# Performance work log

Hardware: AMD Instinct MI355X
Metric: run time of the kernel (lower is better)

The kernel has to match this reference:

```python
import jax, jax.numpy as jnp
import numpy as np

LATENT = 3
HIDDEN = 16
INP = LATENT + 1  # prev_z cat action
B = 1048576


def setup_inputs() -> dict:
    key = jax.random.key(0)
    ks = jax.random.split(key, 11)
    s_ih = 1.0 / np.sqrt(HIDDEN)
    return {
        "prev_z": jax.random.normal(ks[0], (B, LATENT), jnp.float32),
        "action": jax.random.normal(ks[1], (B, 1), jnp.float32),
        "prev_h": jax.random.normal(ks[2], (B, HIDDEN), jnp.float32),
        # GRUCell params (torch layout: [3*H, in] and [3*H, H], gate order r,z,n)
        "W_ih": jax.random.uniform(ks[3], (3 * HIDDEN, INP), jnp.float32, -s_ih, s_ih),
        "W_hh": jax.random.uniform(ks[4], (3 * HIDDEN, HIDDEN), jnp.float32, -s_ih, s_ih),
        "b_ih": jax.random.uniform(ks[5], (3 * HIDDEN,), jnp.float32, -s_ih, s_ih),
        "b_hh": jax.random.uniform(ks[6], (3 * HIDDEN,), jnp.float32, -s_ih, s_ih),
        # prior heads
        "W_mu": jax.random.uniform(ks[7], (LATENT, HIDDEN), jnp.float32, -s_ih, s_ih),
        "b_mu": jax.random.uniform(ks[8], (LATENT,), jnp.float32, -s_ih, s_ih),
        "W_lv": jax.random.uniform(ks[9], (LATENT, HIDDEN), jnp.float32, -s_ih, s_ih),
        "b_lv": jax.random.uniform(ks[10], (LATENT,), jnp.float32, -s_ih, s_ih),
    }


def reference(prev_z, action, prev_h, W_ih, W_hh, b_ih, b_hh, W_mu, b_mu, W_lv, b_lv):
    x = jnp.concatenate([prev_z, action], axis=-1)              # [B, 4]
    gi = x @ W_ih.T + b_ih                                       # [B, 3H]
    gh = prev_h @ W_hh.T + b_hh                                  # [B, 3H]
    i_r, i_z, i_n = jnp.split(gi, 3, axis=-1)
    h_r, h_z, h_n = jnp.split(gh, 3, axis=-1)
    r = jax.nn.sigmoid(i_r + h_r)
    z = jax.nn.sigmoid(i_z + h_z)
    n = jnp.tanh(i_n + r * h_n)
    h = (1.0 - z) * n + z * prev_h                               # [B, H]
    mu = h @ W_mu.T + b_mu                                       # [B, 3]
    logvar = jnp.clip(h @ W_lv.T + b_lv, -5.0, 5.0)              # [B, 3]
    return mu, logvar, h
```

## Files before the change

### kernel.cpp

```cpp
#include <hip/hip_runtime.h>

#define TPB 64
#define WPT 4
#define ROW_DW 20
#define LDS_ROW_F32 (64 * ROW_DW)
#define LDS_MU_F32 192
#define LOG2E 1.44269504088896340736f

typedef _Float16 half8 __attribute__((ext_vector_type(8)));
typedef __fp16  fp16x2 __attribute__((ext_vector_type(2)));
typedef float f32x4 __attribute__((ext_vector_type(4)));

__device__ __forceinline__ half8 pack8(float4 lo, float4 hi) {
    union { fp16x2 p[4]; half8 h; } u;
    u.p[0] = __builtin_amdgcn_cvt_pkrtz(lo.x, lo.y);
    u.p[1] = __builtin_amdgcn_cvt_pkrtz(lo.z, lo.w);
    u.p[2] = __builtin_amdgcn_cvt_pkrtz(hi.x, hi.y);
    u.p[3] = __builtin_amdgcn_cvt_pkrtz(hi.z, hi.w);
    return u.h;
}

__device__ __forceinline__ void nt_store4(float* p, float4 v) {
    union { float4 s; f32x4 e; } u;
    u.s = v;
    __builtin_nontemporal_store(u.e, (f32x4*)p);
}


__global__ __launch_bounds__(64) void prep_kernel(
    const float* __restrict__ W_ih, const float* __restrict__ W_hh,
    const float* __restrict__ b_ih, const float* __restrict__ b_hh,
    const float* __restrict__ W_mu, const float* __restrict__ b_mu,
    const float* __restrict__ W_lv, const float* __restrict__ b_lv,
    void* __restrict__ wsv)
{
    _Float16* wsB = (_Float16*)wsv;
    const int l = threadIdx.x;
    const int col = l & 15, kg = l >> 4;

    #pragma unroll
    for (int t = 0; t < 4; ++t) {
        const int gate = (t == 0) ? col : (t == 1) ? (16 + col) : (32 + col);
        const float scale = (t <= 1) ? -LOG2E : -2.0f * LOG2E;
        #pragma unroll
        for (int i = 0; i < 8; ++i) {
            const int k = kg * 8 + i;
            float v = 0.f;
            if (t <= 1) {
                if (k < 4)       v = W_ih[gate * 4 + k];
                else if (k < 20) v = W_hh[gate * 16 + (k - 4)];
            } else if (t == 2) {
                if (k < 4)       v = W_ih[gate * 4 + k];
            } else {
                if (k >= 4 && k < 20) v = W_hh[gate * 16 + (k - 4)];
            }
            wsB[t * 512 + l * 8 + i] = (_Float16)(v * scale);
        }
    }
    #pragma unroll
    for (int i = 0; i < 8; ++i) {
        const int k = kg * 8 + i;
        wsB[4 * 512 + l * 8 + i] = (_Float16)((k == col + 4) ? 1.f : 0.f);
    }
    #pragma unroll
    for (int i = 0; i < 8; ++i) {
        const int k = kg * 8 + i;
        const int m = col;
        float v = 0.f;
        if (m < 3) {
            if (k < 16)       v = W_mu[m * 16 + k];
            else if (k == 20) v = b_mu[m];
        } else if (m < 6) {
            if (k < 16)       v = W_lv[(m - 3) * 16 + k];
            else if (k == 20) v = b_lv[m - 3];
        }
        wsB[5 * 512 + l * 8 + i] = (_Float16)v;
    }
    if (l < 16) {
        float4* b4 = (float4*)((char*)wsv + 6144);
        b4[l] = make_float4(-LOG2E * (b_ih[l] + b_hh[l]),
                            -LOG2E * (b_ih[16 + l] + b_hh[16 + l]),
                            -2.0f * LOG2E * b_ih[32 + l],
                            -2.0f * LOG2E * b_hh[32 + l]);
    }
}

template<bool EXACT>
__global__ __launch_bounds__(TPB, 4) void rssm_kernel(
    const float* __restrict__ prev_z,
    const float* __restrict__ action,
    const float* __restrict__ prev_h,
    const void*  __restrict__ wsv,
    float* __restrict__ out_mu,
    float* __restrict__ out_lv,
    float* __restrict__ out_h,
    int B)
{
    __shared__ float Wl[LDS_ROW_F32];
    __shared__ float MUl[LDS_MU_F32];
    __shared__ float LVl[LDS_MU_F32];
    const int lane = threadIdx.x;
    const int col = lane & 15, kg = lane >> 4;
    const int wbase = blockIdx.x * 64;
    if (!EXACT && wbase >= B) return;

    float* W  = Wl;
    float* MU = MUl;
    float* LV = LVl;

    const half8* Bp = (const half8*)wsv;
    const half8 bR  = Bp[lane];
    const half8 bZ  = Bp[64 + lane];
    const half8 bNi = Bp[128 + lane];
    const half8 bNh = Bp[192 + lane];
    const half8 bHp = Bp[256 + lane];
    const half8 a2  = Bp[320 + lane];
    const float4 bias = ((const float4*)((const char*)wsv + 6144))[col];

    {
        const float4* hg = (const float4*)prev_h;
        #pragma unroll
        for (int i = 0; i < 4; ++i) {
            const int fi = i * 64 + lane;
            const int r = fi >> 2, w = fi & 3;
            const int gi = EXACT ? (wbase * 4 + fi) : min(wbase * 4 + fi, B * 4 - 1);
            const float4 v = hg[gi];
            *(float4*)&W[r * ROW_DW + 4 + w * 4] = v;
        }
        const int zr = EXACT ? (wbase + lane) : min(wbase + lane, B - 1);
        const float z0 = prev_z[zr * 3 + 0];
        const float z1 = prev_z[zr * 3 + 1];
        const float z2 = prev_z[zr * 3 + 2];
        const float ac = action[zr];
        *(float4*)&W[lane * ROW_DW] = make_float4(z0, z1, z2, ac);
    }

    #pragma unroll
    for (int t = 0; t < WPT; ++t) {
        const float* ap = &W[(t * 16 + col) * ROW_DW + kg * 8];
        const float4 z4 = make_float4(0.f, 0.f, 0.f, 0.f);
        const float4 p0 = (kg < 3) ? *(const float4*)ap : z4;
        const float4 p1 = (kg < 2) ? *(const float4*)(ap + 4) : z4;
        const half8 a = pack8(p0, p1);

        f32x4 accR  = {bias.x, bias.x, bias.x, bias.x};
        f32x4 accZ  = {bias.y, bias.y, bias.y, bias.y};
        f32x4 accNi = {bias.z, bias.z, bias.z, bias.z};
        f32x4 accNh = {bias.w, bias.w, bias.w, bias.w};
        f32x4 accHp = {0.f, 0.f, 0.f, 0.f};
        accR  = __builtin_amdgcn_mfma_f32_16x16x32_f16(a, bR,  accR,  0, 0, 0);
        accZ  = __builtin_amdgcn_mfma_f32_16x16x32_f16(a, bZ,  accZ,  0, 0, 0);
        accNi = __builtin_amdgcn_mfma_f32_16x16x32_f16(a, bNi, accNi, 0, 0, 0);
        accNh = __builtin_amdgcn_mfma_f32_16x16x32_f16(a, bNh, accNh, 0, 0, 0);
        accHp = __builtin_amdgcn_mfma_f32_16x16x32_f16(a, bHp, accHp, 0, 0, 0);

        #pragma unroll
        for (int q = 0; q < 4; ++q) {
            const float r  = __builtin_amdgcn_rcpf(1.0f + __builtin_amdgcn_exp2f(accR[q]));
            const float z  = __builtin_amdgcn_rcpf(1.0f + __builtin_amdgcn_exp2f(accZ[q]));
            const float ta = fmaf(r, accNh[q], accNi[q]);
            const float n  = fmaf(2.0f,
                                  __builtin_amdgcn_rcpf(1.0f + __builtin_amdgcn_exp2f(ta)),
                                  -1.0f);
            const float hv = fmaf(z, accHp[q] - n, n);
            W[(t * 16 + kg * 4 + q) * ROW_DW + 4 + col] = hv;
        }

        half8 b2;
        if (kg < 2) {
            const float* hr = &W[(t * 16 + col) * ROW_DW + 4 + kg * 8];
            b2 = pack8(*(const float4*)hr, *(const float4*)(hr + 4));
        } else {
            #pragma unroll
            for (int i = 0; i < 8; ++i) b2[i] = (_Float16)0.f;
            if (kg == 2) b2[4] = (_Float16)1.0f;
        }
        f32x4 acc2 = {0.f, 0.f, 0.f, 0.f};
        acc2 = __builtin_amdgcn_mfma_f32_16x16x32_f16(a2, b2, acc2, 0, 0, 0);

        const int mr = (t * 16 + col) * 3;
        if (kg == 0) {
            MU[mr + 0] = acc2[0];
            MU[mr + 1] = acc2[1];
            MU[mr + 2] = acc2[2];
            LV[mr + 0] = fminf(fmaxf(acc2[3], -5.0f), 5.0f);
        } else if (kg == 1) {
            LV[mr + 1] = fminf(fmaxf(acc2[0], -5.0f), 5.0f);
            LV[mr + 2] = fminf(fmaxf(acc2[1], -5.0f), 5.0f);
        }

        {
            const int r = lane >> 2, w = lane & 3;
            const float4 hv4 = *(const float4*)&W[(t * 16 + r) * ROW_DW + 4 + w * 4];
            const int orow = wbase + t * 16 + r;
            if (EXACT || orow < B)
                nt_store4(&out_h[(size_t)orow * 16 + w * 4], hv4);
        }
    }

    if (lane < 48) {
        const int gi = wbase * 3 + lane * 4;
        if (EXACT || gi + 3 < B * 3) {
            nt_store4(&out_mu[gi], *(const float4*)&MU[lane * 4]);
            nt_store4(&out_lv[gi], *(const float4*)&LV[lane * 4]);
        }
    }
}

extern "C" void kernel_launch(void* const* d_in, const int* in_sizes, int n_in,
                              void* d_out, int out_size, void* d_ws, size_t ws_size,
                              hipStream_t stream) {
    const float* prev_z = (const float*)d_in[0];
    const float* action = (const float*)d_in[1];
    const float* prev_h = (const float*)d_in[2];
    const float* W_ih   = (const float*)d_in[3];
    const float* W_hh   = (const float*)d_in[4];
    const float* b_ih   = (const float*)d_in[5];
    const float* b_hh   = (const float*)d_in[6];
    const float* W_mu   = (const float*)d_in[7];
    const float* b_mu   = (const float*)d_in[8];
    const float* W_lv   = (const float*)d_in[9];
    const float* b_lv   = (const float*)d_in[10];

    const int B = in_sizes[0] / 3;
    float* out    = (float*)d_out;
    float* out_mu = out;
    float* out_lv = out + (size_t)3 * B;
    float* out_h  = out + (size_t)6 * B;

    prep_kernel<<<1, 64, 0, stream>>>(W_ih, W_hh, b_ih, b_hh,
                                      W_mu, b_mu, W_lv, b_lv, d_ws);

    const int rows_per_block = 64;
    const int blocks = (B + rows_per_block - 1) / rows_per_block;
    if ((B % rows_per_block) == 0)
        rssm_kernel<true><<<blocks, TPB, 0, stream>>>(prev_z, action, prev_h, d_ws,
                                                      out_mu, out_lv, out_h, B);
    else
        rssm_kernel<false><<<blocks, TPB, 0, stream>>>(prev_z, action, prev_h, d_ws,
                                                       out_mu, out_lv, out_h, B);
}
```

Baseline: 41.64 us.

## Process two 64-row chunks per block with async global-to-LDS prefetch of prev_h

Each block now handles 128 rows in two 64-row chunks. prev_h is loaded directly into LDS with global_load_lds, so the second chunk's load overlaps the first chunk's compute. The K layout is reordered to put h first and x last, and x is held as fp16 in a separate LDS buffer, which allows an unpadded 16-float row stride. The cost is half as many blocks, more LDS per block, and manual vmcnt waits; the padding removal may also add LDS bank conflicts.

```diff
diff --git a/kernel.cpp b/kernel.cpp
--- a/kernel.cpp
+++ b/kernel.cpp
@@ -1,13 +1,10 @@
 #include <hip/hip_runtime.h>
 
 #define TPB 64
-#define WPT 4
-#define ROW_DW 20
-#define LDS_ROW_F32 (64 * ROW_DW)
-#define LDS_MU_F32 192
 #define LOG2E 1.44269504088896340736f
 
 typedef _Float16 half8 __attribute__((ext_vector_type(8)));
+typedef _Float16 half4 __attribute__((ext_vector_type(4)));
 typedef __fp16  fp16x2 __attribute__((ext_vector_type(2)));
 typedef float f32x4 __attribute__((ext_vector_type(4)));
 
@@ -19,7 +16,17 @@
     u.p[3] = __builtin_amdgcn_cvt_pkrtz(hi.z, hi.w);
     return u.h;
 }
-
+__device__ __forceinline__ half4 cvt4(float4 v) {
+    union { fp16x2 p[2]; half4 h; } u;
+    u.p[0] = __builtin_amdgcn_cvt_pkrtz(v.x, v.y);
+    u.p[1] = __builtin_amdgcn_cvt_pkrtz(v.z, v.w);
+    return u.h;
+}
+__device__ __forceinline__ half8 cat8(half4 a, half4 b) {
+    union { half4 q[2]; half8 o; } u;
+    u.q[0] = a; u.q[1] = b;
+    return u.o;
+}
 __device__ __forceinline__ void nt_store4(float* p, float4 v) {
     union { float4 s; f32x4 e; } u;
     u.s = v;
@@ -47,12 +54,12 @@
             const int k = kg * 8 + i;
             float v = 0.f;
             if (t <= 1) {
-                if (k < 4)       v = W_ih[gate * 4 + k];
-                else if (k < 20) v = W_hh[gate * 16 + (k - 4)];
+                if (k < 16)            v = W_hh[gate * 16 + k];
+                else if (k < 20)       v = W_ih[gate * 4 + (k - 16)];
             } else if (t == 2) {
-                if (k < 4)       v = W_ih[gate * 4 + k];
+                if (k >= 16 && k < 20) v = W_ih[gate * 4 + (k - 16)];
             } else {
-                if (k >= 4 && k < 20) v = W_hh[gate * 16 + (k - 4)];
+                if (k < 16)            v = W_hh[gate * 16 + k];
             }
             wsB[t * 512 + l * 8 + i] = (_Float16)(v * scale);
         }
@@ -60,7 +67,7 @@
     #pragma unroll
     for (int i = 0; i < 8; ++i) {
         const int k = kg * 8 + i;
-        wsB[4 * 512 + l * 8 + i] = (_Float16)((k == col + 4) ? 1.f : 0.f);
+        wsB[4 * 512 + l * 8 + i] = (_Float16)((k == col) ? 1.f : 0.f);
     }
     #pragma unroll
     for (int i = 0; i < 8; ++i) {
@@ -96,17 +103,14 @@
     float* __restrict__ out_h,
     int B)
 {
-    __shared__ float Wl[LDS_ROW_F32];
-    __shared__ float MUl[LDS_MU_F32];
-    __shared__ float LVl[LDS_MU_F32];
+    __shared__ __align__(16) float Hb[2][64 * 16];
+    __shared__ __align__(8)  _Float16 XAb[64 * 4];
+    __shared__ float MU[192], LV[192];
+
     const int lane = threadIdx.x;
     const int col = lane & 15, kg = lane >> 4;
-    const int wbase = blockIdx.x * 64;
-    if (!EXACT && wbase >= B) return;
-
-    float* W  = Wl;
-    float* MU = MUl;
-    float* LV = LVl;
+    const int bbase = blockIdx.x * 128;
+    if (!EXACT && bbase >= B) return;
 
     const half8* Bp = (const half8*)wsv;
     const half8 bR  = Bp[lane];
@@ -117,92 +121,122 @@
     const half8 a2  = Bp[320 + lane];
     const float4 bias = ((const float4*)((const char*)wsv + 6144))[col];
 
-    {
+    if constexpr (EXACT) {
+        const float4* hg = (const float4*)(prev_h + (size_t)bbase * 16);
+        #pragma unroll
+        for (int c = 0; c < 2; ++c)
+            #pragma unroll
+            for (int i = 0; i < 4; ++i)
+                __builtin_amdgcn_global_load_lds(
+                    (const void*)(hg + c * 256 + i * 64 + lane),
+                    (void*)&Hb[c][i * 256], 16, 0, 0);
+        asm volatile("s_waitcnt vmcnt(4)" ::: "memory");
+        __builtin_amdgcn_sched_barrier(0);
+    } else {
         const float4* hg = (const float4*)prev_h;
         #pragma unroll
-        for (int i = 0; i < 4; ++i) {
-            const int fi = i * 64 + lane;
-            const int r = fi >> 2, w = fi & 3;
-            const int gi = EXACT ? (wbase * 4 + fi) : min(wbase * 4 + fi, B * 4 - 1);
-            const float4 v = hg[gi];
-            *(float4*)&W[r * ROW_DW + 4 + w * 4] = v;
-        }
-        const int zr = EXACT ? (wbase + lane) : min(wbase + lane, B - 1);
-        const float z0 = prev_z[zr * 3 + 0];
-        const float z1 = prev_z[zr * 3 + 1];
-        const float z2 = prev_z[zr * 3 + 2];
-        const float ac = action[zr];
-        *(float4*)&W[lane * ROW_DW] = make_float4(z0, z1, z2, ac);
-    }
-
-    #pragma unroll
-    for (int t = 0; t < WPT; ++t) {
-        const float* ap = &W[(t * 16 + col) * ROW_DW + kg * 8];
-        const float4 z4 = make_float4(0.f, 0.f, 0.f, 0.f);
-        const float4 p0 = (kg < 3) ? *(const float4*)ap : z4;
-        const float4 p1 = (kg < 2) ? *(const float4*)(ap + 4) : z4;
-        const half8 a = pack8(p0, p1);
-
-        f32x4 accR  = {bias.x, bias.x, bias.x, bias.x};
-        f32x4 accZ  = {bias.y, bias.y, bias.y, bias.y};
-        f32x4 accNi = {bias.z, bias.z, bias.z, bias.z};
-        f32x4 accNh = {bias.w, bias.w, bias.w, bias.w};
-        f32x4 accHp = {0.f, 0.f, 0.f, 0.f};
-        accR  = __builtin_amdgcn_mfma_f32_16x16x32_f16(a, bR,  accR,  0, 0, 0);
-        accZ  = __builtin_amdgcn_mfma_f32_16x16x32_f16(a, bZ,  accZ,  0, 0, 0);
-        accNi = __builtin_amdgcn_mfma_f32_16x16x32_f16(a, bNi, accNi, 0, 0, 0);
-        accNh = __builtin_amdgcn_mfma_f32_16x16x32_f16(a, bNh, accNh, 0, 0, 0);
-        accHp = __builtin_amdgcn_mfma_f32_16x16x32_f16(a, bHp, accHp, 0, 0, 0);
-
-        #pragma unroll
-        for (int q = 0; q < 4; ++q) {
-            const float r  = __builtin_amdgcn_rcpf(1.0f + __builtin_amdgcn_exp2f(accR[q]));
-            const float z  = __builtin_amdgcn_rcpf(1.0f + __builtin_amdgcn_exp2f(accZ[q]));
-            const float ta = fmaf(r, accNh[q], accNi[q]);
-            const float n  = fmaf(2.0f,
-                                  __builtin_amdgcn_rcpf(1.0f + __builtin_amdgcn_exp2f(ta)),
-                                  -1.0f);
-            const float hv = fmaf(z, accHp[q] - n, n);
-            W[(t * 16 + kg * 4 + q) * ROW_DW + 4 + col] = hv;
-        }
-
-        half8 b2;
-        if (kg < 2) {
-            const float* hr = &W[(t * 16 + col) * ROW_DW + 4 + kg * 8];
-            b2 = pack8(*(const float4*)hr, *(const float4*)(hr + 4));
-        } else {
+        for (int c = 0; c < 2; ++c)
             #pragma unroll
-            for (int i = 0; i < 8; ++i) b2[i] = (_Float16)0.f;
-            if (kg == 2) b2[4] = (_Float16)1.0f;
-        }
-        f32x4 acc2 = {0.f, 0.f, 0.f, 0.f};
-        acc2 = __builtin_amdgcn_mfma_f32_16x16x32_f16(a2, b2, acc2, 0, 0, 0);
-
-        const int mr = (t * 16 + col) * 3;
-        if (kg == 0) {
-            MU[mr + 0] = acc2[0];
-            MU[mr + 1] = acc2[1];
-            MU[mr + 2] = acc2[2];
-            LV[mr + 0] = fminf(fmaxf(acc2[3], -5.0f), 5.0f);
-        } else if (kg == 1) {
-            LV[mr + 1] = fminf(fmaxf(acc2[0], -5.0f), 5.0f);
-            LV[mr + 2] = fminf(fmaxf(acc2[1], -5.0f), 5.0f);
-        }
-
-        {
-            const int r = lane >> 2, w = lane & 3;
-            const float4 hv4 = *(const float4*)&W[(t * 16 + r) * ROW_DW + 4 + w * 4];
-            const int orow = wbase + t * 16 + r;
-            if (EXACT || orow < B)
-                nt_store4(&out_h[(size_t)orow * 16 + w * 4], hv4);
-        }
-    }
-
-    if (lane < 48) {
-        const int gi = wbase * 3 + lane * 4;
-        if (EXACT || gi + 3 < B * 3) {
-            nt_store4(&out_mu[gi], *(const float4*)&MU[lane * 4]);
-            nt_store4(&out_lv[gi], *(const float4*)&LV[lane * 4]);
+            for (int i = 0; i < 4; ++i) {
+                const int gi = min(bbase * 4 + c * 256 + i * 64 + lane, B * 4 - 1);
+                *(float4*)&Hb[c][i * 256 + lane * 4] = hg[gi];
+            }
+    }
+
+    half4 zz; zz[0] = zz[1] = zz[2] = zz[3] = (_Float16)0.f;
+
+    #pragma unroll
+    for (int c = 0; c < 2; ++c) {
+        const int cbase = bbase + c * 64;
+        if (EXACT || cbase < B) {
+            if (EXACT && c == 1) {
+                asm volatile("s_waitcnt vmcnt(0)" ::: "memory");
+                __builtin_amdgcn_sched_barrier(0);
+            }
+            float* Hc = Hb[c];
+
+            {
+                const int zr = EXACT ? (cbase + lane) : min(cbase + lane, B - 1);
+                *(half4*)&XAb[lane * 4] =
+                    cvt4(make_float4(prev_z[zr * 3 + 0], prev_z[zr * 3 + 1],
+                                     prev_z[zr * 3 + 2], action[zr]));
+            }
+
+            #pragma unroll
+            for (int t = 0; t < 4; ++t) {
+                half8 a;
+                if (kg < 2) {
+                    const float4 p0 = *(const float4*)&Hc[(t * 16 + col) * 16 + kg * 8];
+                    const float4 p1 = *(const float4*)&Hc[(t * 16 + col) * 16 + kg * 8 + 4];
+                    a = pack8(p0, p1);
+                } else if (kg == 2) {
+                    a = cat8(*(const half4*)&XAb[(t * 16 + col) * 4], zz);
+                } else {
+                    a = cat8(zz, zz);
+                }
+
+                f32x4 accR  = {bias.x, bias.x, bias.x, bias.x};
+                f32x4 accZ  = {bias.y, bias.y, bias.y, bias.y};
+                f32x4 accNi = {bias.z, bias.z, bias.z, bias.z};
+                f32x4 accNh = {bias.w, bias.w, bias.w, bias.w};
+                f32x4 accHp = {0.f, 0.f, 0.f, 0.f};
+                accR  = __builtin_amdgcn_mfma_f32_16x16x32_f16(a, bR,  accR,  0, 0, 0);
+                accZ  = __builtin_amdgcn_mfma_f32_16x16x32_f16(a, bZ,  accZ,  0, 0, 0);
+                accNi = __builtin_amdgcn_mfma_f32_16x16x32_f16(a, bNi, accNi, 0, 0, 0);
+                accNh = __builtin_amdgcn_mfma_f32_16x16x32_f16(a, bNh, accNh, 0, 0, 0);
+                accHp = __builtin_amdgcn_mfma_f32_16x16x32_f16(a, bHp, accHp, 0, 0, 0);
+
+                #pragma unroll
+                for (int q = 0; q < 4; ++q) {
+                    const float r  = __builtin_amdgcn_rcpf(1.0f + __builtin_amdgcn_exp2f(accR[q]));
+                    const float z  = __builtin_amdgcn_rcpf(1.0f + __builtin_amdgcn_exp2f(accZ[q]));
+                    const float ta = fmaf(r, accNh[q], accNi[q]);
+                    const float n  = fmaf(2.0f,
+                                          __builtin_amdgcn_rcpf(1.0f + __builtin_amdgcn_exp2f(ta)),
+                                          -1.0f);
+                    const float hv = fmaf(z, accHp[q] - n, n);
+                    Hc[(t * 16 + kg * 4 + q) * 16 + col] = hv;
+                }
+
+                half8 b2;
+                if (kg < 2) {
+                    const float4 h0 = *(const float4*)&Hc[(t * 16 + col) * 16 + kg * 8];
+                    const float4 h1 = *(const float4*)&Hc[(t * 16 + col) * 16 + kg * 8 + 4];
+                    b2 = pack8(h0, h1);
+                } else {
+                    b2 = cat8(zz, zz);
+                    if (kg == 2) b2[4] = (_Float16)1.0f;
+                }
+                f32x4 acc2 = {0.f, 0.f, 0.f, 0.f};
+                acc2 = __builtin_amdgcn_mfma_f32_16x16x32_f16(a2, b2, acc2, 0, 0, 0);
+
+                const int mr = (t * 16 + col) * 3;
+                if (kg == 0) {
+                    MU[mr + 0] = acc2[0];
+                    MU[mr + 1] = acc2[1];
+                    MU[mr + 2] = acc2[2];
+                    LV[mr + 0] = fminf(fmaxf(acc2[3], -5.0f), 5.0f);
+                } else if (kg == 1) {
+                    LV[mr + 1] = fminf(fmaxf(acc2[0], -5.0f), 5.0f);
+                    LV[mr + 2] = fminf(fmaxf(acc2[1], -5.0f), 5.0f);
+                }
+
+                {
+                    const int r = lane >> 2, w = lane & 3;
+                    const float4 hv4 = *(const float4*)&Hc[(t * 16 + r) * 16 + w * 4];
+                    const int orow = cbase + t * 16 + r;
+                    if (EXACT || orow < B)
+                        nt_store4(&out_h[(size_t)orow * 16 + w * 4], hv4);
+                }
+            }
+
+            if (lane < 48) {
+                const int gi = cbase * 3 + lane * 4;
+                if (EXACT || gi + 3 < B * 3) {
+                    nt_store4(&out_mu[gi], *(const float4*)&MU[lane * 4]);
+                    nt_store4(&out_lv[gi], *(const float4*)&LV[lane * 4]);
+                }
+            }
         }
     }
 }
@@ -231,7 +265,7 @@
     prep_kernel<<<1, 64, 0, stream>>>(W_ih, W_hh, b_ih, b_hh,
                                       W_mu, b_mu, W_lv, b_lv, d_ws);
 
-    const int rows_per_block = 64;
+    const int rows_per_block = 128;
     const int blocks = (B + rows_per_block - 1) / rows_per_block;
     if ((B % rows_per_block) == 0)
         rssm_kernel<true><<<blocks, TPB, 0, stream>>>(prev_z, action, prev_h, d_ws,
```

Measured after the change: 41.51 us. No clear change (-0.3%).
